# Kernel optimization log

Measured on AMD Instinct MI355X. Metric: run time of the kernel, lower is better.

The kernel has to match this reference:

```python
import jax, jax.numpy as jnp
import numpy as np

N = 20000
E = 320000
IN = 512
H = 4
C = 128
ED = 4
NEG_SLOPE = 0.2
BN_EPS = 1e-5


def setup_inputs() -> dict:
    key = jax.random.key(0)
    ks = jax.random.split(key, 10)
    x = jax.random.normal(ks[0], (N, IN), dtype=jnp.float32)
    edge_index = jax.random.randint(ks[1], (2, E), 0, N, dtype=jnp.int64)
    edge_attr = jax.random.normal(ks[2], (E, ED), dtype=jnp.float32)
    # GATConv params (glorot-ish scaling)
    W = jax.random.normal(ks[3], (IN, H * C), dtype=jnp.float32) / np.sqrt(IN)
    W_edge = jax.random.normal(ks[4], (ED, H * C), dtype=jnp.float32) / np.sqrt(ED)
    att_src = jax.random.normal(ks[5], (H, C), dtype=jnp.float32) / np.sqrt(C)
    att_dst = jax.random.normal(ks[6], (H, C), dtype=jnp.float32) / np.sqrt(C)
    att_edge = jax.random.normal(ks[7], (H, C), dtype=jnp.float32) / np.sqrt(C)
    bias = jnp.zeros((H * C,), dtype=jnp.float32)
    gamma = jnp.ones((H * C,), dtype=jnp.float32)
    beta = jnp.zeros((H * C,), dtype=jnp.float32)
    return {"x": x, "edge_index": edge_index, "edge_attr": edge_attr,
            "W": W, "W_edge": W_edge, "att_src": att_src, "att_dst": att_dst,
            "att_edge": att_edge, "bias": bias, "gamma": gamma, "beta": beta}


def _edge_gat(x, edge_index, edge_attr, W, W_edge, att_src, att_dst, att_edge,
              bias, gamma, beta):
    n = x.shape[0]
    # PyG default: add self loops, edge_attr fill_value='mean'
    loop = jnp.arange(n, dtype=edge_index.dtype)
    src = jnp.concatenate([edge_index[0], loop])  # [E+N]
    dst = jnp.concatenate([edge_index[1], loop])
    ea = jnp.concatenate(
        [edge_attr, jnp.broadcast_to(edge_attr.mean(0), (n, edge_attr.shape[1]))], 0)

    h = (x @ W).reshape(n, H, C)                       # [N,H,C]
    a_src = (h * att_src[None]).sum(-1)                # [N,H]
    a_dst = (h * att_dst[None]).sum(-1)                # [N,H]
    e = (ea @ W_edge).reshape(-1, H, C)                # [E+N,H,C]
    a_edge = (e * att_edge[None]).sum(-1)              # [E+N,H]

    alpha = a_src[src] + a_dst[dst] + a_edge           # [E+N,H]
    alpha = jax.nn.leaky_relu(alpha, NEG_SLOPE)
    # segment softmax over edges grouped by target node
    amax = jax.lax.stop_gradient(jax.ops.segment_max(alpha, dst, num_segments=n))
    ex = jnp.exp(alpha - amax[dst])
    denom = jax.ops.segment_sum(ex, dst, num_segments=n)
    att = ex / (denom[dst] + 1e-16)                    # [E+N,H]

    msg = h[src] * att[:, :, None]                     # [E+N,H,C]
    out = jax.ops.segment_sum(msg, dst, num_segments=n).reshape(n, H * C) + bias

    # BatchNorm1d in training mode: batch statistics, biased variance
    mu = out.mean(0)
    var = out.var(0)
    return (out - mu) / jnp.sqrt(var + BN_EPS) * gamma + beta


def reference(x, edge_index, edge_attr, W, W_edge, att_src, att_dst, att_edge,
              bias, gamma, beta):
    return _edge_gat(x, edge_index, edge_attr, W, W_edge, att_src, att_dst,
                     att_edge, bias, gamma, beta)
```

## Files before the change

### kernel.cpp

```cpp
#include <hip/hip_runtime.h>
#include <math.h>

#define N_NODES 20000
#define N_EDGES 320000
#define TOT_E   340000
#define IN_F    512
#define HC      512
#define NHEAD   4
#define CHAN    128
#define NEG_SLOPE 0.2f
#define BN_EPS  1e-5f

#define GEMM_BM 32

#define PACK_BLOCKS 128
#define PREP_BLOCKS 256

#define BN_BLOCKS 157
#define BN_ROWS2 128
#define NSLICE 4

typedef short short8v __attribute__((ext_vector_type(8)));
typedef float f32x4  __attribute__((ext_vector_type(4)));
typedef unsigned short u16x8 __attribute__((ext_vector_type(8)));
typedef unsigned short u16x4 __attribute__((ext_vector_type(4)));

__device__ __forceinline__ unsigned short f2bf(float f) {
  unsigned u = __float_as_uint(f);
  return (unsigned short)((u + 0x7FFFu + ((u >> 16) & 1u)) >> 16);
}
__device__ __forceinline__ float bf2f(unsigned short b) {
  return __uint_as_float(((unsigned)b) << 16);
}

__global__ void prep_pack_kernel(const float* __restrict__ W,
                                 unsigned short* __restrict__ Bp,
                                 const float* __restrict__ EA, const int* __restrict__ EI,
                                 const float* __restrict__ We, const float* __restrict__ aedg,
                                 float* __restrict__ msum, int* __restrict__ deg,
                                 float* __restrict__ qm) {
  if (blockIdx.x < PACK_BLOCKS) {
    const int tid = blockIdx.x * blockDim.x + threadIdx.x;
    const int l = tid & 63;
    const int k32 = (tid >> 6) & 15;
    const int n16 = tid >> 10;
    const int col = n16 * 16 + (l & 15);
    const int k = k32 * 32 + ((l >> 4) << 3);
    unsigned short v[8];
#pragma unroll
    for (int j = 0; j < 8; ++j) v[j] = f2bf(W[(size_t)(k + j) * HC + col]);
    *(short8v*)&Bp[(size_t)tid * 8] = *(short8v*)v;
  } else {
    const int bid = blockIdx.x - PACK_BLOCKS;
    if (bid < 16 && threadIdx.x < 64) {
      const int d = bid >> 2, h = bid & 3, lane = threadIdx.x;
      const int base = h * CHAN + lane * 2;
      float v = We[d * HC + base] * aedg[base] + We[d * HC + base + 1] * aedg[base + 1];
#pragma unroll
      for (int m = 32; m >= 1; m >>= 1) v += __shfl_down(v, m);
      if (lane == 0) qm[d * 4 + h] = v;
    }
    float s0 = 0.f, s1 = 0.f, s2 = 0.f, s3 = 0.f;
    for (int i = bid * blockDim.x + threadIdx.x; i < N_EDGES;
         i += PREP_BLOCKS * blockDim.x) {
      const float4 v = *(const float4*)&EA[(size_t)i * 4];
      s0 += v.x; s1 += v.y; s2 += v.z; s3 += v.w;
      atomicAdd(&deg[EI[N_EDGES + i]], 1);
    }
#pragma unroll
    for (int m = 32; m >= 1; m >>= 1) {
      s0 += __shfl_down(s0, m); s1 += __shfl_down(s1, m);
      s2 += __shfl_down(s2, m); s3 += __shfl_down(s3, m);
    }
    __shared__ float red[4][4];
    const int lane = threadIdx.x & 63, wid = threadIdx.x >> 6;
    if (lane == 0) { red[wid][0] = s0; red[wid][1] = s1; red[wid][2] = s2; red[wid][3] = s3; }
    __syncthreads();
    if (threadIdx.x < 4) {
      float v = red[0][threadIdx.x] + red[1][threadIdx.x] + red[2][threadIdx.x] + red[3][threadIdx.x];
      atomicAdd(&msum[threadIdx.x], v);
    }
  }
}

__global__ __launch_bounds__(1024) void scan_kernel(const int* __restrict__ deg,
                                                    int* __restrict__ rowstart) {
  __shared__ int part[1024];
  const int t = threadIdx.x;
  const int base = t * 20;
  int local[20];
  int s = 0;
#pragma unroll
  for (int i = 0; i < 20; ++i) {
    const int idx = base + i;
    const int v = (idx < N_NODES) ? deg[idx] : 0;
    local[i] = s;
    s += v;
  }
  part[t] = s;
  __syncthreads();
  for (int off = 1; off < 1024; off <<= 1) {
    const int v = (t >= off) ? part[t - off] : 0;
    __syncthreads();
    part[t] += v;
    __syncthreads();
  }
  const int excl = (t > 0) ? part[t - 1] : 0;
#pragma unroll
  for (int i = 0; i < 20; ++i) {
    const int idx = base + i;
    if (idx < N_NODES) rowstart[idx] = excl + local[i];
  }
  if (t == 1023) rowstart[N_NODES] = part[1023];
}

__global__ __launch_bounds__(256) void gemm_direct_fused(
    const float* __restrict__ X, const unsigned short* __restrict__ Bp_,
    const float* __restrict__ att_s, const float* __restrict__ att_d,
    unsigned short* __restrict__ H16, float* __restrict__ a_src,
    float* __restrict__ a_dst) {
  __shared__ unsigned short As[2][GEMM_BM * 64];
  const short8v* __restrict__ Bp = (const short8v*)Bp_;
  const int tid = threadIdx.x;
  const int l = tid & 63;
  const int w = tid >> 6;
  const int bm = blockIdx.x * GEMM_BM;
  const int srow = tid >> 3;
  const int skc = (tid & 7) * 8;
  const int sidx = srow * 64 + (skc ^ ((srow & 7) << 3));
  const float* __restrict__ xrow = &X[(size_t)(bm + srow) * IN_F];
  const int fr = l & 15;
  const int fg = l >> 4;
  const int cl = l & 15;
  const short8v* __restrict__ bbase = Bp + (size_t)(w * 8) * 16 * 64 + l;
  f32x4 acc[2][8] = {};
  float4 f0 = *(const float4*)&xrow[skc];
  float4 f1 = *(const float4*)&xrow[skc + 4];
  {
    unsigned short vv[8] = {f2bf(f0.x), f2bf(f0.y), f2bf(f0.z), f2bf(f0.w),
                            f2bf(f1.x), f2bf(f1.y), f2bf(f1.z), f2bf(f1.w)};
    *(short8v*)&As[0][sidx] = *(short8v*)vv;
  }
  short8v bcur[8];
#pragma unroll
  for (int n = 0; n < 8; ++n) bcur[n] = bbase[(size_t)(n * 16) * 64];
  f0 = *(const float4*)&xrow[64 + skc];
  f1 = *(const float4*)&xrow[64 + skc + 4];
#pragma unroll
  for (int t = 0; t < 8; ++t) {
    __syncthreads();
    if (t < 7) {
      unsigned short vv[8] = {f2bf(f0.x), f2bf(f0.y), f2bf(f0.z), f2bf(f0.w),
                              f2bf(f1.x), f2bf(f1.y), f2bf(f1.z), f2bf(f1.w)};
      *(short8v*)&As[(t + 1) & 1][sidx] = *(short8v*)vv;
      if (t < 6) {
        f0 = *(const float4*)&xrow[(t + 2) * 64 + skc];
        f1 = *(const float4*)&xrow[(t + 2) * 64 + skc + 4];
      }
    }
#pragma unroll
    for (int ks = 0; ks < 2; ++ks) {
      const int kk = t * 2 + ks;
      short8v bnxt[8];
      if (kk < 15) {
#pragma unroll
        for (int n = 0; n < 8; ++n) bnxt[n] = bbase[(size_t)(n * 16 + kk + 1) * 64];
      }
      short8v a[2];
#pragma unroll
      for (int m = 0; m < 2; ++m)
        a[m] = *(const short8v*)
            &As[t & 1][(m * 16 + fr) * 64 + ((ks * 32 + fg * 8) ^ ((fr & 7) << 3))];
#pragma unroll
      for (int n = 0; n < 8; ++n) {
        acc[0][n] = __builtin_amdgcn_mfma_f32_16x16x32_bf16(a[0], bcur[n], acc[0][n], 0, 0, 0);
        acc[1][n] = __builtin_amdgcn_mfma_f32_16x16x32_bf16(a[1], bcur[n], acc[1][n], 0, 0, 0);
      }
      if (kk < 15) {
#pragma unroll
        for (int n = 0; n < 8; ++n) bcur[n] = bnxt[n];
      }
    }
  }
  const int rbase = fg * 4;
#pragma unroll
  for (int m = 0; m < 2; ++m) {
#pragma unroll
    for (int r = 0; r < 4; ++r) {
      const int row = bm + m * 16 + rbase + r;
#pragma unroll
      for (int n = 0; n < 8; ++n)
        H16[(size_t)row * HC + (w * 8 + n) * 16 + cl] = f2bf(acc[m][n][r]);
    }
  }
  float as_v[8], ad_v[8];
#pragma unroll
  for (int n = 0; n < 8; ++n) {
    const int c = w * CHAN + n * 16 + cl;
    as_v[n] = att_s[c];
    ad_v[n] = att_d[c];
  }
#pragma unroll
  for (int m = 0; m < 2; ++m) {
#pragma unroll
    for (int r = 0; r < 4; ++r) {
      float ps = 0.f, pd = 0.f;
#pragma unroll
      for (int n = 0; n < 8; ++n) { ps += acc[m][n][r] * as_v[n]; pd += acc[m][n][r] * ad_v[n]; }
#pragma unroll
      for (int mask = 1; mask <= 8; mask <<= 1) {
        ps += __shfl_xor(ps, mask); pd += __shfl_xor(pd, mask);
      }
      if (cl == 0) {
        const int row = bm + m * 16 + rbase + r;
        a_src[row * 4 + w] = ps;
        a_dst[row * 4 + w] = pd;
      }
    }
  }
}

__global__ void scatter_alpha_kernel(const int* __restrict__ EI, const float* __restrict__ EA,
                                     const int* __restrict__ rowstart, int* __restrict__ cnt,
                                     const float* __restrict__ a_src, const float* __restrict__ a_dst,
                                     const float* __restrict__ msum, const float* __restrict__ q,
                                     float* __restrict__ recs) {
  const int k = blockIdx.x * blockDim.x + threadIdx.x;
  if (k >= TOT_E) return;
  int s, d, pos;
  float e0, e1, e2, e3;
  if (k < N_EDGES) {
    s = EI[k]; d = EI[N_EDGES + k];
    const float4 e = *(const float4*)&EA[(size_t)k * 4];
    e0 = e.x; e1 = e.y; e2 = e.z; e3 = e.w;
    pos = rowstart[d] + atomicAdd(&cnt[d], 1);
  } else {
    s = d = k - N_EDGES;
    const float inv = 1.0f / (float)N_EDGES;
    e0 = msum[0] * inv; e1 = msum[1] * inv; e2 = msum[2] * inv; e3 = msum[3] * inv;
    pos = k;
  }
  const float4 as = *(const float4*)&a_src[s * 4];
  const float4 ad = *(const float4*)&a_dst[d * 4];
  const float asv[4] = {as.x, as.y, as.z, as.w};
  const float adv[4] = {ad.x, ad.y, ad.z, ad.w};
  float al[4];
#pragma unroll
  for (int h = 0; h < 4; ++h) {
    float ae = e0 * q[h] + e1 * q[4 + h] + e2 * q[8 + h] + e3 * q[12 + h];
    float a = asv[h] + adv[h] + ae;
    al[h] = (a >= 0.f) ? a : NEG_SLOPE * a;
  }
  float4 lo = {al[0], al[1], al[2], al[3]};
  float4 hi = {__int_as_float(s), 0.f, 0.f, 0.f};
  *(float4*)&recs[(size_t)pos * 8] = lo;
  *(float4*)&recs[(size_t)pos * 8 + 4] = hi;
}

__global__ __launch_bounds__(256) void agg_fused_kernel(
    const int* __restrict__ rowstart, const float* __restrict__ recs,
    const unsigned short* __restrict__ H16, unsigned short* __restrict__ o16) {
  const int wid = threadIdx.x >> 6;
  const int n = blockIdx.x * 4 + wid;
  const int l = threadIdx.x & 63;
  const int head = l >> 4;
  const int j = l * 8;
  const int beg = rowstart[n], end = rowstart[n + 1];
  float m = recs[(size_t)(N_EDGES + n) * 8 + head];
  float den = 1.0f;
  const u16x8 hv = *(const u16x8*)&H16[(size_t)n * HC + j];
  float acc[8];
#pragma unroll
  for (int c = 0; c < 8; ++c) acc[c] = bf2f(hv[c]);
  int s_nxt = 0;
  float a_nxt = 0.f;
  if (beg < end) {
    s_nxt = __float_as_int(recs[(size_t)beg * 8 + 4]);
    a_nxt = recs[(size_t)beg * 8 + head];
  }
  for (int idx = beg; idx < end; ++idx) {
    const int s = s_nxt;
    const float a = a_nxt;
    if (idx + 1 < end) {
      s_nxt = __float_as_int(recs[(size_t)(idx + 1) * 8 + 4]);
      a_nxt = recs[(size_t)(idx + 1) * 8 + head];
    }
    const u16x8 v = *(const u16x8*)&H16[(size_t)s * HC + j];
    if (a <= m) {
      const float wgt = __expf(a - m);
      den += wgt;
#pragma unroll
      for (int c = 0; c < 8; ++c) acc[c] += wgt * bf2f(v[c]);
    } else {
      const float r = __expf(m - a);
      den = den * r + 1.0f;
#pragma unroll
      for (int c = 0; c < 8; ++c) acc[c] = acc[c] * r + bf2f(v[c]);
      m = a;
    }
  }
  const float dinv = 1.0f / (den + 1e-16f);
  unsigned short ov[8];
#pragma unroll
  for (int c = 0; c < 8; ++c) ov[c] = f2bf(acc[c] * dinv);
  *(short8v*)&o16[(size_t)n * HC + j] = *(short8v*)ov;
}

__global__ __launch_bounds__(256) void bn_stats16_kernel(
    const unsigned short* __restrict__ o16,
    float* __restrict__ psum, float* __restrict__ psq) {
  __shared__ float sv[4][HC];
  const int rg = threadIdx.x >> 6;
  const int cg = threadIdx.x & 63;
  const int j = cg * 8;
  const int rend0 = blockIdx.x * BN_ROWS2 + BN_ROWS2;
  const int rend = (rend0 < N_NODES) ? rend0 : N_NODES;
  float ssum[8] = {0.f, 0.f, 0.f, 0.f, 0.f, 0.f, 0.f, 0.f};
  float ssq[8]  = {0.f, 0.f, 0.f, 0.f, 0.f, 0.f, 0.f, 0.f};
  for (int r = blockIdx.x * BN_ROWS2 + rg; r < rend; r += 4) {
    const u16x8 v = *(const u16x8*)&o16[(size_t)r * HC + j];
#pragma unroll
    for (int c = 0; c < 8; ++c) {
      const float a = bf2f(v[c]);
      ssum[c] += a;
      ssq[c] += a * a;
    }
  }
  const int t = threadIdx.x;
  const int slice = (blockIdx.x & (NSLICE - 1)) * HC;
#pragma unroll
  for (int c = 0; c < 8; ++c) sv[rg][j + c] = ssum[c];
  __syncthreads();
  const float r0 = sv[0][t] + sv[1][t] + sv[2][t] + sv[3][t];
  const float r1 = sv[0][t + 256] + sv[1][t + 256] + sv[2][t + 256] + sv[3][t + 256];
  __syncthreads();
#pragma unroll
  for (int c = 0; c < 8; ++c) sv[rg][j + c] = ssq[c];
  __syncthreads();
  const float q0 = sv[0][t] + sv[1][t] + sv[2][t] + sv[3][t];
  const float q1 = sv[0][t + 256] + sv[1][t + 256] + sv[2][t + 256] + sv[3][t + 256];
  atomicAdd(&psum[slice + t], r0);
  atomicAdd(&psum[slice + t + 256], r1);
  atomicAdd(&psq[slice + t], q0);
  atomicAdd(&psq[slice + t + 256], q1);
}

__global__ void bn_apply_kernel(const unsigned short* __restrict__ o16,
                                const float* __restrict__ psum, const float* __restrict__ psq,
                                const float* __restrict__ gamma, const float* __restrict__ beta,
                                float* __restrict__ out) {
  const int i = blockIdx.x * blockDim.x + threadIdx.x;
  if (i >= N_NODES * HC / 4) return;
  const int j4 = (i & (HC / 4 - 1)) * 4;
  float4 cs = *(const float4*)&psum[j4];
  float4 cq = *(const float4*)&psq[j4];
#pragma unroll
  for (int sl = 1; sl < NSLICE; ++sl) {
    const float4 a = *(const float4*)&psum[sl * HC + j4];
    const float4 b = *(const float4*)&psq[sl * HC + j4];
    cs.x += a.x; cs.y += a.y; cs.z += a.z; cs.w += a.w;
    cq.x += b.x; cq.y += b.y; cq.z += b.z; cq.w += b.w;
  }
  const float4 g  = *(const float4*)&gamma[j4];
  const float4 b  = *(const float4*)&beta[j4];
  const float inv = 1.0f / N_NODES;
  const float mux = cs.x * inv, muy = cs.y * inv, muz = cs.z * inv, muw = cs.w * inv;
  const float scx = g.x * rsqrtf(cq.x * inv - mux * mux + BN_EPS);
  const float scy = g.y * rsqrtf(cq.y * inv - muy * muy + BN_EPS);
  const float scz = g.z * rsqrtf(cq.z * inv - muz * muz + BN_EPS);
  const float scw = g.w * rsqrtf(cq.w * inv - muw * muw + BN_EPS);
  const u16x4 v16 = *(const u16x4*)&o16[(size_t)i * 4];
  float4 v;
  v.x = (bf2f(v16[0]) - mux) * scx + b.x;
  v.y = (bf2f(v16[1]) - muy) * scy + b.y;
  v.z = (bf2f(v16[2]) - muz) * scz + b.z;
  v.w = (bf2f(v16[3]) - muw) * scw + b.w;
  ((float4*)out)[i] = v;
}

extern "C" void kernel_launch(void* const* d_in, const int* in_sizes, int n_in,
                              void* d_out, int out_size, void* d_ws, size_t ws_size,
                              hipStream_t stream) {
  const float* x     = (const float*)d_in[0];
  const int*   ei    = (const int*)d_in[1];
  const float* ea    = (const float*)d_in[2];
  const float* W     = (const float*)d_in[3];
  const float* We    = (const float*)d_in[4];
  const float* att_s = (const float*)d_in[5];
  const float* att_d = (const float*)d_in[6];
  const float* att_e = (const float*)d_in[7];
  const float* gamma = (const float*)d_in[9];
  const float* beta  = (const float*)d_in[10];
  float* out = (float*)d_out;
  float* ws  = (float*)d_ws;

  unsigned short* H16     = (unsigned short*)ws;
  float*    a_src   = (float*)(H16 + (size_t)N_NODES * HC);
  float*    a_dst   = a_src + N_NODES * NHEAD;
  float*    recs    = a_dst + N_NODES * NHEAD;
  float*    qm      = recs + (size_t)TOT_E * 8;
  int*      rowstart= (int*)(qm + 16);
  unsigned short* Bp  = (unsigned short*)(rowstart + 20004);
  unsigned short* o16 = Bp + (size_t)32 * 16 * 64 * 8;
  int*      deg     = (int*)(o16 + (size_t)N_NODES * HC);
  int*      cnt     = deg + N_NODES;
  float*    msum    = (float*)(cnt + N_NODES);
  float*    psum    = msum + 4;
  float*    psq     = psum + NSLICE * HC;

  const size_t zero_bytes =
      (size_t)(N_NODES * 2 + 4 + NSLICE * HC * 2) * sizeof(float);
  hipMemsetAsync(deg, 0, zero_bytes, stream);

  prep_pack_kernel<<<PACK_BLOCKS + PREP_BLOCKS, 256, 0, stream>>>(
      W, Bp, ea, ei, We, att_e, msum, deg, qm);
  scan_kernel<<<1, 1024, 0, stream>>>(deg, rowstart);
  gemm_direct_fused<<<N_NODES / GEMM_BM, 256, 0, stream>>>(x, Bp, att_s, att_d,
                                                           H16, a_src, a_dst);
  scatter_alpha_kernel<<<(TOT_E + 255) / 256, 256, 0, stream>>>(ei, ea, rowstart, cnt,
                                                                a_src, a_dst, msum, qm,
                                                                recs);
  agg_fused_kernel<<<N_NODES / 4, 256, 0, stream>>>(rowstart, recs, H16, o16);
  bn_stats16_kernel<<<BN_BLOCKS, 256, 0, stream>>>(o16, psum, psq);
  bn_apply_kernel<<<(N_NODES * HC / 4 + 255) / 256, 256, 0, stream>>>(o16, psum, psq,
                                                                      gamma, beta, out);
}
```

Before: 168.3 us.

## Fold prefix scan into GEMM launch as extra block; split aggregation into four launches

Removes the standalone single-block scan kernel and runs the degree prefix-sum in one extra block (index 625) of the GEMM grid, so one launch and its serial dependency go away and the scan overlaps with GEMM work. The scan now uses 256 threads with 79 elements each and reads deg twice. Separately, the aggregation kernel is split into four launches over quarter node ranges via a node_base offset. That adds launch overhead and may serve as a probe of per-chunk behaviour. The extra GEMM block executes the scan serially per thread, which could lengthen the tail if it is scheduled last.

```diff
diff --git a/kernel.cpp b/kernel.cpp
--- a/kernel.cpp
+++ b/kernel.cpp
@@ -83,42 +83,37 @@
   }
 }
 
-__global__ __launch_bounds__(1024) void scan_kernel(const int* __restrict__ deg,
-                                                    int* __restrict__ rowstart) {
-  __shared__ int part[1024];
-  const int t = threadIdx.x;
-  const int base = t * 20;
-  int local[20];
-  int s = 0;
-#pragma unroll
-  for (int i = 0; i < 20; ++i) {
-    const int idx = base + i;
-    const int v = (idx < N_NODES) ? deg[idx] : 0;
-    local[i] = s;
-    s += v;
-  }
-  part[t] = s;
-  __syncthreads();
-  for (int off = 1; off < 1024; off <<= 1) {
-    const int v = (t >= off) ? part[t - off] : 0;
-    __syncthreads();
-    part[t] += v;
-    __syncthreads();
-  }
-  const int excl = (t > 0) ? part[t - 1] : 0;
-#pragma unroll
-  for (int i = 0; i < 20; ++i) {
-    const int idx = base + i;
-    if (idx < N_NODES) rowstart[idx] = excl + local[i];
-  }
-  if (t == 1023) rowstart[N_NODES] = part[1023];
-}
-
 __global__ __launch_bounds__(256) void gemm_direct_fused(
     const float* __restrict__ X, const unsigned short* __restrict__ Bp_,
     const float* __restrict__ att_s, const float* __restrict__ att_d,
     unsigned short* __restrict__ H16, float* __restrict__ a_src,
-    float* __restrict__ a_dst) {
+    float* __restrict__ a_dst, const int* __restrict__ deg,
+    int* __restrict__ rowstart) {
+  if (blockIdx.x == 625) {
+    __shared__ int part[256];
+    const int t = threadIdx.x;
+    const int base = t * 79;
+    int s = 0;
+    for (int i = 0; i < 79; ++i) {
+      const int idx = base + i;
+      if (idx < N_NODES) s += deg[idx];
+    }
+    part[t] = s;
+    __syncthreads();
+    for (int off = 1; off < 256; off <<= 1) {
+      const int v = (t >= off) ? part[t - off] : 0;
+      __syncthreads();
+      part[t] += v;
+      __syncthreads();
+    }
+    int excl = (t > 0) ? part[t - 1] : 0;
+    for (int i = 0; i < 79; ++i) {
+      const int idx = base + i;
+      if (idx < N_NODES) { rowstart[idx] = excl; excl += deg[idx]; }
+    }
+    if (t == 255) rowstart[N_NODES] = part[255];
+    return;
+  }
   __shared__ unsigned short As[2][GEMM_BM * 64];
   const short8v* __restrict__ Bp = (const short8v*)Bp_;
   const int tid = threadIdx.x;
@@ -259,9 +254,10 @@
 
 __global__ __launch_bounds__(256) void agg_fused_kernel(
     const int* __restrict__ rowstart, const float* __restrict__ recs,
-    const unsigned short* __restrict__ H16, unsigned short* __restrict__ o16) {
+    const unsigned short* __restrict__ H16, unsigned short* __restrict__ o16,
+    int node_base) {
   const int wid = threadIdx.x >> 6;
-  const int n = blockIdx.x * 4 + wid;
+  const int n = node_base + blockIdx.x * 4 + wid;
   const int l = threadIdx.x & 63;
   const int head = l >> 4;
   const int j = l * 8;
@@ -414,13 +410,16 @@
 
   prep_pack_kernel<<<PACK_BLOCKS + PREP_BLOCKS, 256, 0, stream>>>(
       W, Bp, ea, ei, We, att_e, msum, deg, qm);
-  scan_kernel<<<1, 1024, 0, stream>>>(deg, rowstart);
-  gemm_direct_fused<<<N_NODES / GEMM_BM, 256, 0, stream>>>(x, Bp, att_s, att_d,
-                                                           H16, a_src, a_dst);
+  gemm_direct_fused<<<N_NODES / GEMM_BM + 1, 256, 0, stream>>>(x, Bp, att_s, att_d,
+                                                               H16, a_src, a_dst,
+                                                               deg, rowstart);
   scatter_alpha_kernel<<<(TOT_E + 255) / 256, 256, 0, stream>>>(ei, ea, rowstart, cnt,
                                                                 a_src, a_dst, msum, qm,
                                                                 recs);
-  agg_fused_kernel<<<N_NODES / 4, 256, 0, stream>>>(rowstart, recs, H16, o16);
+  agg_fused_kernel<<<N_NODES / 16, 256, 0, stream>>>(rowstart, recs, H16, o16, 0);
+  agg_fused_kernel<<<N_NODES / 16, 256, 0, stream>>>(rowstart, recs, H16, o16, 5000);
+  agg_fused_kernel<<<N_NODES / 16, 256, 0, stream>>>(rowstart, recs, H16, o16, 10000);
+  agg_fused_kernel<<<N_NODES / 16, 256, 0, stream>>>(rowstart, recs, H16, o16, 15000);
   bn_stats16_kernel<<<BN_BLOCKS, 256, 0, stream>>>(o16, psum, psq);
   bn_apply_kernel<<<(N_NODES * HC / 4 + 255) / 256, 256, 0, stream>>>(o16, psum, psq,
                                                                       gamma, beta, out);
```

After: 199.1 us. 1.18x slower.
